# Kernel tuning notes

Hardware: AMD Instinct MI355X
Metric: run time of the kernel (lower is better)

## Reference

```python
import jax, jax.numpy as jnp
import numpy as np

B, L, D, H, M = 2, 512, 1024, 16, 16384
HD = D // H  # 64


def setup_inputs() -> dict:
    key = jax.random.key(0)
    ks = jax.random.split(key, 8)
    s = 0.02
    return {
        "x": jax.random.normal(ks[0], (B, L, D), dtype=jnp.float32),
        "mem_keys": jax.random.normal(ks[1], (M, HD), dtype=jnp.float32),
        "mem_values": jax.random.normal(ks[2], (M, HD), dtype=jnp.float32),
        "Wq": jax.random.normal(ks[3], (D, D), dtype=jnp.float32) * s,
        "bq": jnp.zeros((D,), jnp.float32),
        "Wk": jax.random.normal(ks[4], (D, D), dtype=jnp.float32) * s,
        "bk": jnp.zeros((D,), jnp.float32),
        "Wv": jax.random.normal(ks[5], (D, D), dtype=jnp.float32) * s,
        "bv": jnp.zeros((D,), jnp.float32),
        "Wo": jax.random.normal(ks[6], (D, D), dtype=jnp.float32) * s,
        "bo": jnp.zeros((D,), jnp.float32),
        "top_k": 8,
    }


def reference(x, mem_keys, mem_values, Wq, bq, Wk, bk, Wv, bv, Wo, bo, top_k):
    b, l, d = x.shape
    h, hd = H, d // H
    # Q/K/V projections -> [B, L, H, HD]
    q = (x @ Wq.T + bq).reshape(b, l, h, hd)
    k = (x @ Wk.T + bk).reshape(b, l, h, hd)
    v = (x @ Wv.T + bv).reshape(b, l, h, hd)

    # exact inner-product top-k memory search (FAISS equivalent) per (b, l, h) query
    q_flat = q.reshape(b * l * h, hd)
    sim = q_flat @ mem_keys.T                      # [B*L*H, M]
    idx = jax.lax.top_k(sim, top_k)[1]             # [B*L*H, K]
    # gather retrieved KV, lay out as memory-prefix along seq: [B, L*K, H, HD]
    m_k = mem_keys[idx].reshape(b, l, h, top_k, hd).transpose(0, 1, 3, 2, 4).reshape(b, l * top_k, h, hd)
    m_v = mem_values[idx].reshape(b, l, h, top_k, hd).transpose(0, 1, 3, 2, 4).reshape(b, l * top_k, h, hd)

    k_full = jnp.concatenate([m_k, k], axis=1)     # [B, Lm+L, H, HD]
    v_full = jnp.concatenate([m_v, v], axis=1)
    lm = l * top_k

    scale = 1.0 / np.sqrt(hd)
    scores = jnp.einsum("blhd,bmhd->bhlm", q, k_full) * scale
    # memory prefix always visible; local part causal (flash_attn bottom-right causal)
    i = jnp.arange(l)[:, None]
    j = jnp.arange(lm + l)[None, :]
    mask = (j < lm) | ((j - lm) <= i)              # [L, Lm+L]
    neg = jnp.finfo(scores.dtype).min
    attn = jax.nn.softmax(jnp.where(mask, scores, neg), axis=-1)
    out = jnp.einsum("bhlm,bmhd->blhd", attn, v_full).reshape(b, l, d)
    return out @ Wo.T + bo
```

## Files before the change

### kernel.cpp

```cpp
#include <hip/hip_runtime.h>

typedef __bf16 bf16_t;
typedef __bf16 bf16x8 __attribute__((ext_vector_type(8)));
typedef __bf16 bf16x4 __attribute__((ext_vector_type(4)));
typedef __bf16 bf16x2 __attribute__((ext_vector_type(2)));
typedef float f32x4 __attribute__((ext_vector_type(4)));

#define DEV __device__ __forceinline__
#define MFMA16 __builtin_amdgcn_mfma_f32_16x16x32_bf16

constexpr int Bb = 2, Ls = 512, Dd = 1024, Hh = 16, HD = 64, Mm = 16384, TK = 8;
constexpr int KSPLIT = 4;
constexpr int CAP = 40;
constexpr int NQ = Bb * Ls * Hh;
constexpr int CH = 3;

constexpr size_t OFF_QF   = 0;
constexpr size_t OFF_KF   = OFF_QF + (size_t)NQ * HD;
constexpr size_t OFF_VF   = OFF_KF + (size_t)NQ * HD;
constexpr size_t OFF_QH   = OFF_VF + (size_t)NQ * HD;
constexpr size_t OFF_QL   = OFF_QH + (size_t)NQ * HD / 2;
constexpr size_t OFF_KHG  = OFF_QL + (size_t)NQ * HD / 2;
constexpr size_t OFF_FCAND = OFF_KHG + (size_t)Mm * HD / 2;
constexpr size_t OFF_FCNT  = OFF_FCAND + (size_t)KSPLIT * NQ * CAP;
constexpr size_t OFF_F8   = OFF_FCNT + (size_t)KSPLIT * NQ;
constexpr size_t OFF_ML   = OFF_F8 + (size_t)NQ * TK;
constexpr size_t OFF_PA   = OFF_ML + (size_t)CH * NQ * 2;
constexpr size_t WS_ELEMS = OFF_PA + (size_t)CH * NQ * HD + 16;
constexpr size_t WS_BYTES = WS_ELEMS * 4;

DEV void ld8f(const float* p, float* dst) {
  float4 a = *(const float4*)p, b = *(const float4*)(p + 4);
  dst[0]=a.x; dst[1]=a.y; dst[2]=a.z; dst[3]=a.w;
  dst[4]=b.x; dst[5]=b.y; dst[6]=b.z; dst[7]=b.w;
}

DEV void split8(const float* av, bf16x8& hi, bf16x8& lo) {
#pragma unroll
  for (int j = 0; j < 8; ++j) {
    bf16_t h_ = (bf16_t)av[j];
    hi[j] = h_;
    lo[j] = (bf16_t)(av[j] - (float)h_);
  }
}

DEV bf16x8 ld8h(const bf16_t* p) {
  bf16x4 a = *(const bf16x4*)p;
  bf16x4 b = *(const bf16x4*)(p + 4);
  bf16x8 r;
#pragma unroll
  for (int i = 0; i < 4; ++i) { r[i] = a[i]; r[i + 4] = b[i]; }
  return r;
}

__global__ __launch_bounds__(256) void ws_sentinel(float* __restrict__ out, int n, float v) {
  int i = blockIdx.x * 256 + threadIdx.x;
  if (i < n) out[i] = v;
}

__global__ __launch_bounds__(256) void prep_keys(const float* __restrict__ mk,
                                                 bf16_t* __restrict__ khg) {
  const size_t i = ((size_t)blockIdx.x * 256 + threadIdx.x) * 8;
  float v[8]; ld8f(mk + i, v);
  bf16x8 h;
#pragma unroll
  for (int j = 0; j < 8; ++j) h[j] = (bf16_t)v[j];
  *(bf16x8*)(khg + i) = h;
}

__global__ __launch_bounds__(256) void qkv_mfma(
    const float* __restrict__ x,
    const float* __restrict__ Wq, const float* __restrict__ bq,
    const float* __restrict__ Wk, const float* __restrict__ bk,
    const float* __restrict__ Wv, const float* __restrict__ bv,
    float* __restrict__ qf, bf16_t* __restrict__ qh, bf16_t* __restrict__ ql,
    float* __restrict__ kf, float* __restrict__ vf) {
  const int z = blockIdx.z;
  const float* W    = (z == 0) ? Wq : ((z == 1) ? Wk : Wv);
  const float* bias = (z == 0) ? bq : ((z == 1) ? bk : bv);
  const int tid = threadIdx.x;
  const int lane = tid & 63, wv = tid >> 6;
  const int l15 = lane & 15, quad = lane >> 4;
  const int mrow = blockIdx.x * 64 + wv * 16 + l15;
  const int ncol0 = blockIdx.y * 64;
  f32x4 acc[4] = {};
  const size_t abase = (size_t)mrow * Dd + quad * 8;
  for (int kk = 0; kk < Dd; kk += 32) {
    float av[8]; ld8f(x + abase + kk, av);
    bf16x8 ahi, alo; split8(av, ahi, alo);
#pragma unroll
    for (int t = 0; t < 4; ++t) {
      float bv8[8]; ld8f(W + (size_t)(ncol0 + t * 16 + l15) * Dd + kk + quad * 8, bv8);
      bf16x8 bhi, blo; split8(bv8, bhi, blo);
      acc[t] = MFMA16(ahi, bhi, acc[t], 0, 0, 0);
      acc[t] = MFMA16(alo, bhi, acc[t], 0, 0, 0);
      acc[t] = MFMA16(ahi, blo, acc[t], 0, 0, 0);
    }
  }
#pragma unroll
  for (int t = 0; t < 4; ++t) {
    int col = ncol0 + t * 16 + l15;
    int h = col >> 6, hd = col & 63;
    float bb = bias[col];
#pragma unroll
    for (int r = 0; r < 4; ++r) {
      int row = blockIdx.x * 64 + wv * 16 + quad * 4 + r;
      int b = row >> 9, l = row & 511;
      float val = acc[t][r] + bb;
      size_t o = ((size_t)(b * Hh + h) * Ls + l) * HD + hd;
      if (z == 0) {
        qf[o] = val;
        bf16_t hv = (bf16_t)val;
        qh[o] = hv;
        ql[o] = (bf16_t)(val - (float)hv);
      } else if (z == 1) {
        kf[o] = val;
      } else {
        vf[o] = val;
      }
    }
  }
}

__global__ __launch_bounds__(256, 5) void topk_thresh(
    const bf16_t* __restrict__ qh, const bf16_t* __restrict__ khg,
    int* __restrict__ fcand, int* __restrict__ fcnt) {
  __shared__ __align__(16) float  W8[4][64][8];
  __shared__ float Tarr[64];
  __shared__ int   cntq[64];
  __shared__ int   Cand[64][CAP];

  const int tid = threadIdx.x;
  const int lane = tid & 63, w = tid >> 6;
  const int l15 = lane & 15, quad = lane >> 4;
  const int qbase = blockIdx.x * 64;
  const int split = blockIdx.y;
  const int key0 = split * (Mm / KSPLIT);
  constexpr int NT = (Mm / KSPLIT) / 64;

  bf16x8 bq[4][2];
#pragma unroll
  for (int g = 0; g < 4; ++g) {
    const bf16_t* qp = qh + (size_t)(qbase + g * 16 + l15) * HD + quad * 8;
    bq[g][0] = *(const bf16x8*)qp;
    bq[g][1] = *(const bf16x8*)(qp + 32);
  }

  const bf16_t* kbase = khg + (size_t)(key0 + w * 16 + l15) * HD + quad * 8;

  float s8[8];
#pragma unroll
  for (int r = 0; r < 8; ++r) s8[r] = -3.0e38f;

  bf16x8 a0 = *(const bf16x8*)(kbase);
  bf16x8 a1 = *(const bf16x8*)(kbase + 32);
  for (int tile = 0; tile < NT; ++tile) {
    const bf16_t* np = kbase + (size_t)((tile + 1 < NT) ? tile + 1 : 0) * (64 * HD);
    bf16x8 n0 = *(const bf16x8*)(np);
    bf16x8 n1 = *(const bf16x8*)(np + 32);
    float keep = -3.0e38f;
#pragma unroll
    for (int g = 0; g < 4; ++g) {
      f32x4 acc = {0.f, 0.f, 0.f, 0.f};
      acc = MFMA16(a0, bq[g][0], acc, 0, 0, 0);
      acc = MFMA16(a1, bq[g][1], acc, 0, 0, 0);
      float v = fmaxf(fmaxf(acc[0], acc[1]), fmaxf(acc[2], acc[3]));
      v = fmaxf(v, __shfl_xor(v, 16));
      v = fmaxf(v, __shfl_xor(v, 32));
      if (g == quad) keep = v;
    }
    if (keep > s8[7]) {
      s8[7] = keep;
#pragma unroll
      for (int p = 7; p > 0; --p)
        if (s8[p] > s8[p - 1]) { float t = s8[p]; s8[p] = s8[p - 1]; s8[p - 1] = t; }
    }
    a0 = n0; a1 = n1;
  }
  {
    float* dst = &W8[w][quad * 16 + l15][0];
#pragma unroll
    for (int r = 0; r < 8; ++r) dst[r] = s8[r];
  }
  __syncthreads();
  if (tid < 64) {
    float t8[8];
#pragma unroll
    for (int r = 0; r < 8; ++r) t8[r] = -3.0e38f;
#pragma unroll
    for (int wv2 = 0; wv2 < 4; ++wv2) {
      float4 u0 = *(const float4*)&W8[wv2][tid][0];
      float4 u1 = *(const float4*)&W8[wv2][tid][4];
      float vals[8] = {u0.x, u0.y, u0.z, u0.w, u1.x, u1.y, u1.z, u1.w};
#pragma unroll
      for (int r = 0; r < 8; ++r) {
        float v = vals[r];
        if (v > t8[7]) {
          t8[7] = v;
#pragma unroll
          for (int p = 7; p > 0; --p)
            if (t8[p] > t8[p - 1]) { float tt = t8[p]; t8[p] = t8[p - 1]; t8[p - 1] = tt; }
        }
      }
    }
    Tarr[tid] = t8[7];
    cntq[tid] = 0;
  }
  __syncthreads();
  float Tq[4];
#pragma unroll
  for (int g = 0; g < 4; ++g) Tq[g] = Tarr[g * 16 + l15];

  a0 = *(const bf16x8*)(kbase);
  a1 = *(const bf16x8*)(kbase + 32);
  for (int tile = 0; tile < NT; ++tile) {
    const bf16_t* np = kbase + (size_t)((tile + 1 < NT) ? tile + 1 : 0) * (64 * HD);
    bf16x8 n0 = *(const bf16x8*)(np);
    bf16x8 n1 = *(const bf16x8*)(np + 32);
#pragma unroll
    for (int g = 0; g < 4; ++g) {
      f32x4 acc = {0.f, 0.f, 0.f, 0.f};
      acc = MFMA16(a0, bq[g][0], acc, 0, 0, 0);
      acc = MFMA16(a1, bq[g][1], acc, 0, 0, 0);
      const int kb = key0 + tile * 64 + w * 16 + quad * 4;
      const int qq = g * 16 + l15;
#pragma unroll
      for (int r = 0; r < 4; ++r) {
        if (acc[r] >= Tq[g]) {
          int pos = atomicAdd(&cntq[qq], 1);
          if (pos < CAP) Cand[qq][pos] = kb + r;
        }
      }
    }
    a0 = n0; a1 = n1;
  }
  __syncthreads();
  if (tid < 64) {
    int c = cntq[tid];
    fcnt[(size_t)split * NQ + qbase + tid] = (c < CAP) ? c : CAP;
  }
  for (int i = tid; i < 64 * CAP; i += 256) {
    int q = i / CAP, s = i - q * CAP;
    fcand[((size_t)split * NQ + qbase + q) * CAP + s] = Cand[q][s];
  }
}

__global__ __launch_bounds__(64) void rescore8(
    const float* __restrict__ qf, const float* __restrict__ mk,
    const int* __restrict__ fcand, const int* __restrict__ fcnt,
    int* __restrict__ f8) {
  const int qid = blockIdx.x * 64 + threadIdx.x;
  float q[64];
#pragma unroll
  for (int c = 0; c < 16; ++c) {
    float4 v4 = *(const float4*)(qf + (size_t)qid * HD + 4 * c);
    q[4*c]=v4.x; q[4*c+1]=v4.y; q[4*c+2]=v4.z; q[4*c+3]=v4.w;
  }
  float sc[TK]; int id[TK];
#pragma unroll
  for (int r = 0; r < TK; ++r) { sc[r] = -3.0e38f; id[r] = 0x7fffffff; }
#pragma unroll 1
  for (int sp = 0; sp < KSPLIT; ++sp) {
    int cnt = fcnt[(size_t)sp * NQ + qid];
    if (cnt > CAP) cnt = CAP;
#pragma unroll 1
    for (int c = 0; c < cnt; ++c) {
      int kidx = fcand[((size_t)sp * NQ + qid) * CAP + c] & (Mm - 1);
      const float4* kr = (const float4*)(mk + (size_t)kidx * HD);
      float a0 = 0, a1 = 0, a2 = 0, a3 = 0;
#pragma unroll
      for (int cc = 0; cc < 16; ++cc) {
        float4 kv = kr[cc];
        a0 += q[4*cc]*kv.x; a1 += q[4*cc+1]*kv.y; a2 += q[4*cc+2]*kv.z; a3 += q[4*cc+3]*kv.w;
      }
      float s = (a0 + a1) + (a2 + a3);
      if (s > sc[TK - 1] || (s == sc[TK - 1] && kidx < id[TK - 1])) {
        sc[TK - 1] = s; id[TK - 1] = kidx;
#pragma unroll
        for (int p = TK - 1; p > 0; --p) {
          bool sw = (sc[p] > sc[p - 1]) || (sc[p] == sc[p - 1] && id[p] < id[p - 1]);
          if (sw) {
            float ts = sc[p]; sc[p] = sc[p - 1]; sc[p - 1] = ts;
            int   ti = id[p]; id[p] = id[p - 1]; id[p - 1] = ti;
          }
        }
      }
    }
  }
#pragma unroll
  for (int r = 0; r < TK; ++r) f8[(size_t)qid * TK + r] = id[r] & (Mm - 1);
}

__global__ __launch_bounds__(256) void flash_mfma(
    const bf16_t* __restrict__ qh, const bf16_t* __restrict__ ql,
    const float* __restrict__ kf, const float* __restrict__ vf,
    const float* __restrict__ mk, const float* __restrict__ mv,
    const int* __restrict__ f8, float* __restrict__ ml, float* __restrict__ pacc) {
  __shared__ __align__(16) bf16_t KH[64][72];
  __shared__ __align__(16) bf16_t KL[64][72];
  __shared__ __align__(16) bf16_t VTH[64][68];
  __shared__ __align__(16) bf16_t VTL[64][68];
  __shared__ __align__(16) bf16_t PH[64][72];
  __shared__ __align__(16) bf16_t PL[64][72];

  const int tid = threadIdx.x;
  const int lane = tid & 63, w = tid >> 6;
  const int l15 = lane & 15, quad = lane >> 4;
  const int qt = blockIdx.x, bh = blockIdx.y, chunk = blockIdx.z;
  const int il = qt * 64 + w * 16 + l15;
  const int qid = bh * Ls + il;
  const bf16x8 qh0 = *(const bf16x8*)(qh + (size_t)qid * HD + quad * 8);
  const bf16x8 qh1 = *(const bf16x8*)(qh + (size_t)qid * HD + 32 + quad * 8);
  const bf16x8 ql0 = *(const bf16x8*)(ql + (size_t)qid * HD + quad * 8);
  const bf16x8 ql1 = *(const bf16x8*)(ql + (size_t)qid * HD + 32 + quad * 8);

  f32x4 O[4] = {};
  float m = -3.0e38f, lsum = 0.f;
  const float scale = 0.125f;
  const int tbase = chunk * 24;
  const int nmem  = (chunk == 2) ? 16 : 24;
  const int ntiles = (chunk == 2) ? 17 + qt : 24;
  const int skey = tid >> 2, spart = tid & 3;
  const int kpair = tid & 31, dgroup = tid >> 5;

  float kreg[16], va[8], vb[8];
  auto stage_load = [&](int t) {
    const float *ks, *vsa, *vsb;
    if (chunk == 2 && t >= nmem) {
      int jlK = (t - nmem) * 64 + skey;
      ks = kf + ((size_t)bh * Ls + jlK) * HD + spart * 16;
      int jlV = (t - nmem) * 64 + 2 * kpair;
      vsa = vf + ((size_t)bh * Ls + jlV) * HD + dgroup * 8;
      vsb = vsa + HD;
    } else {
      int jgK = (tbase + t) * 64 + skey;
      int sK = f8[((size_t)bh * Ls + (jgK >> 3)) * TK + (jgK & 7)] & (Mm - 1);
      ks = mk + (size_t)sK * HD + spart * 16;
      int jgV = (tbase + t) * 64 + 2 * kpair;
      int2 s2 = *(const int2*)(f8 + ((size_t)bh * Ls + (jgV >> 3)) * TK + (jgV & 7));
      vsa = mv + (size_t)(s2.x & (Mm - 1)) * HD + dgroup * 8;
      vsb = mv + (size_t)(s2.y & (Mm - 1)) * HD + dgroup * 8;
    }
    ld8f(ks, kreg); ld8f(ks + 8, kreg + 8);
    ld8f(vsa, va);
    ld8f(vsb, vb);
  };
  stage_load(0);

  for (int tile = 0; tile < ntiles; ++tile) {
    const bool local_tile = (chunk == 2) && (tile >= nmem);
    __syncthreads();
    {
      bf16x8 h0, l0, h1, l1;
      split8(kreg, h0, l0); split8(kreg + 8, h1, l1);
      *(bf16x8*)&KH[skey][spart * 16]     = h0;
      *(bf16x8*)&KH[skey][spart * 16 + 8] = h1;
      *(bf16x8*)&KL[skey][spart * 16]     = l0;
      *(bf16x8*)&KL[skey][spart * 16 + 8] = l1;
#pragma unroll
      for (int j = 0; j < 8; ++j) {
        bf16_t ha = (bf16_t)va[j]; bf16_t la = (bf16_t)(va[j] - (float)ha);
        bf16_t hb = (bf16_t)vb[j]; bf16_t lb = (bf16_t)(vb[j] - (float)hb);
        const int d = dgroup * 8 + j;
        bf16x2 th; th[0] = ha; th[1] = hb;
        bf16x2 tl; tl[0] = la; tl[1] = lb;
        *(bf16x2*)&VTH[d][2 * kpair] = th;
        *(bf16x2*)&VTL[d][2 * kpair] = tl;
      }
    }
    __syncthreads();
    if (tile + 1 < ntiles) stage_load(tile + 1);

    f32x4 S[4];
    __builtin_amdgcn_s_setprio(1);
#pragma unroll
    for (int sub = 0; sub < 4; ++sub) {
      const bf16x8 ah0 = *(const bf16x8*)&KH[sub * 16 + l15][quad * 8];
      const bf16x8 ah1 = *(const bf16x8*)&KH[sub * 16 + l15][32 + quad * 8];
      const bf16x8 al0 = *(const bf16x8*)&KL[sub * 16 + l15][quad * 8];
      const bf16x8 al1 = *(const bf16x8*)&KL[sub * 16 + l15][32 + quad * 8];
      f32x4 acc = {0.f, 0.f, 0.f, 0.f};
      acc = MFMA16(ah0, qh0, acc, 0, 0, 0);
      acc = MFMA16(ah1, qh1, acc, 0, 0, 0);
      acc = MFMA16(al0, qh0, acc, 0, 0, 0);
      acc = MFMA16(al1, qh1, acc, 0, 0, 0);
      acc = MFMA16(ah0, ql0, acc, 0, 0, 0);
      acc = MFMA16(ah1, ql1, acc, 0, 0, 0);
#pragma unroll
      for (int r = 0; r < 4; ++r) {
        float sv = acc[r] * scale;
        if (local_tile && ((tile - nmem) * 64 + sub * 16 + quad * 4 + r) > il) sv = -3.0e38f;
        S[sub][r] = sv;
      }
    }
    __builtin_amdgcn_s_setprio(0);
    float tm = -3.0e38f;
#pragma unroll
    for (int sub = 0; sub < 4; ++sub)
#pragma unroll
      for (int r = 0; r < 4; ++r) tm = fmaxf(tm, S[sub][r]);
    tm = fmaxf(tm, __shfl_xor(tm, 16));
    tm = fmaxf(tm, __shfl_xor(tm, 32));
    float mnew = fmaxf(m, tm);
    float alpha = __expf(m - mnew);
    lsum *= alpha;
#pragma unroll
    for (int t = 0; t < 4; ++t) O[t] *= alpha;
    m = mnew;
#pragma unroll
    for (int sub = 0; sub < 4; ++sub) {
      bf16_t ph4[4], pl4[4];
#pragma unroll
      for (int r = 0; r < 4; ++r) {
        float p = __expf(S[sub][r] - mnew);
        lsum += p;
        bf16_t hv = (bf16_t)p;
        ph4[r] = hv;
        pl4[r] = (bf16_t)(p - (float)hv);
      }
      *(uint2*)&PH[w * 16 + l15][sub * 16 + quad * 4] = *(uint2*)ph4;
      *(uint2*)&PL[w * 16 + l15][sub * 16 + quad * 4] = *(uint2*)pl4;
    }
    const bf16x8 ph0 = *(const bf16x8*)&PH[w * 16 + l15][quad * 8];
    const bf16x8 ph1 = *(const bf16x8*)&PH[w * 16 + l15][32 + quad * 8];
    const bf16x8 pl0 = *(const bf16x8*)&PL[w * 16 + l15][quad * 8];
    const bf16x8 pl1 = *(const bf16x8*)&PL[w * 16 + l15][32 + quad * 8];
    __builtin_amdgcn_s_setprio(1);
#pragma unroll
    for (int t = 0; t < 4; ++t) {
      const bf16x8 vh0 = ld8h(&VTH[t * 16 + l15][quad * 8]);
      const bf16x8 vh1 = ld8h(&VTH[t * 16 + l15][32 + quad * 8]);
      const bf16x8 vl0 = ld8h(&VTL[t * 16 + l15][quad * 8]);
      const bf16x8 vl1 = ld8h(&VTL[t * 16 + l15][32 + quad * 8]);
      O[t] = MFMA16(vh0, ph0, O[t], 0, 0, 0);
      O[t] = MFMA16(vh1, ph1, O[t], 0, 0, 0);
      O[t] = MFMA16(vl0, ph0, O[t], 0, 0, 0);
      O[t] = MFMA16(vl1, ph1, O[t], 0, 0, 0);
      O[t] = MFMA16(vh0, pl0, O[t], 0, 0, 0);
      O[t] = MFMA16(vh1, pl1, O[t], 0, 0, 0);
    }
    __builtin_amdgcn_s_setprio(0);
  }
  lsum += __shfl_xor(lsum, 16);
  lsum += __shfl_xor(lsum, 32);
  if (quad == 0) {
    ml[((size_t)chunk * NQ + qid) * 2 + 0] = m;
    ml[((size_t)chunk * NQ + qid) * 2 + 1] = lsum;
  }
  float* pa = pacc + ((size_t)chunk * NQ + qid) * 64;
#pragma unroll
  for (int t = 0; t < 4; ++t) {
    float4 v4; v4.x = O[t][0]; v4.y = O[t][1]; v4.z = O[t][2]; v4.w = O[t][3];
    *(float4*)(pa + t * 16 + quad * 4) = v4;
  }
}

__global__ __launch_bounds__(256) void oproj_comb(
    const float* __restrict__ ml, const float* __restrict__ pacc,
    const float* __restrict__ Wo, const float* __restrict__ bo,
    float* __restrict__ out) {
  const int tid = threadIdx.x;
  const int lane = tid & 63, wv = tid >> 6;
  const int l15 = lane & 15, quad = lane >> 4;
  const int mrow = blockIdx.x * 64 + wv * 16 + l15;
  const int b = mrow >> 9, l = mrow & 511;
  const int ncol0 = blockIdx.y * 64;
  f32x4 acc[4] = {};
  for (int kk = 0; kk < Dd; kk += 32) {
    const int h = kk >> 6;
    const size_t qid = (size_t)(b * Hh + h) * Ls + l;
    float m0 = ml[qid * 2 + 0],                    l0 = ml[qid * 2 + 1];
    float m1 = ml[((size_t)NQ + qid) * 2 + 0],     l1 = ml[((size_t)NQ + qid) * 2 + 1];
    float m2 = ml[((size_t)2 * NQ + qid) * 2 + 0], l2 = ml[((size_t)2 * NQ + qid) * 2 + 1];
    float M = fmaxf(m0, fmaxf(m1, m2));
    float w0 = __expf(m0 - M), w1 = __expf(m1 - M), w2 = __expf(m2 - M);
    float inv = 1.f / (w0 * l0 + w1 * l1 + w2 * l2);
    const int d0 = (kk & 63) + quad * 8;
    float a0v[8], a1v[8], a2v[8], av[8];
    ld8f(pacc + qid * 64 + d0, a0v);
    ld8f(pacc + ((size_t)NQ + qid) * 64 + d0, a1v);
    ld8f(pacc + ((size_t)2 * NQ + qid) * 64 + d0, a2v);
#pragma unroll
    for (int j = 0; j < 8; ++j) av[j] = (w0 * a0v[j] + w1 * a1v[j] + w2 * a2v[j]) * inv;
    bf16x8 ahi, alo; split8(av, ahi, alo);
#pragma unroll
    for (int t = 0; t < 4; ++t) {
      float wv8[8]; ld8f(Wo + (size_t)(ncol0 + t * 16 + l15) * Dd + kk + quad * 8, wv8);
      bf16x8 whi, wlo; split8(wv8, whi, wlo);
      acc[t] = MFMA16(ahi, whi, acc[t], 0, 0, 0);
      acc[t] = MFMA16(alo, whi, acc[t], 0, 0, 0);
      acc[t] = MFMA16(ahi, wlo, acc[t], 0, 0, 0);
    }
  }
#pragma unroll
  for (int t = 0; t < 4; ++t) {
    int col = ncol0 + t * 16 + l15;
    float bb = bo[col];
#pragma unroll
    for (int r = 0; r < 4; ++r) {
      int row = blockIdx.x * 64 + wv * 16 + quad * 4 + r;
      out[(size_t)row * Dd + col] = acc[t][r] + bb;
    }
  }
}

extern "C" void kernel_launch(void* const* d_in, const int* in_sizes, int n_in,
                              void* d_out, int out_size, void* d_ws, size_t ws_size,
                              hipStream_t stream) {
  (void)in_sizes; (void)n_in;
  const float* x  = (const float*)d_in[0];
  const float* mk = (const float*)d_in[1];
  const float* mv = (const float*)d_in[2];
  const float* Wq = (const float*)d_in[3];
  const float* bq = (const float*)d_in[4];
  const float* Wk = (const float*)d_in[5];
  const float* bk = (const float*)d_in[6];
  const float* Wv = (const float*)d_in[7];
  const float* bv = (const float*)d_in[8];
  const float* Wo = (const float*)d_in[9];
  const float* bo = (const float*)d_in[10];
  float* ws = (float*)d_ws;

  if (ws_size < WS_BYTES) {
    float v = (float)(ws_size >> 20) + 0.5f;
    ws_sentinel<<<(out_size + 255) / 256, 256, 0, stream>>>((float*)d_out, out_size, v);
    return;
  }

  float*  QF    = ws + OFF_QF;
  float*  KF    = ws + OFF_KF;
  float*  VF    = ws + OFF_VF;
  bf16_t* QH    = (bf16_t*)(ws + OFF_QH);
  bf16_t* QL    = (bf16_t*)(ws + OFF_QL);
  bf16_t* KHG   = (bf16_t*)(ws + OFF_KHG);
  int*    FCAND = (int*)(ws + OFF_FCAND);
  int*    FCNT  = (int*)(ws + OFF_FCNT);
  int*    F8    = (int*)(ws + OFF_F8);
  float*  ML    = ws + OFF_ML;
  float*  PA    = ws + OFF_PA;

  prep_keys<<<(Mm * HD) / (256 * 8), 256, 0, stream>>>(mk, KHG);
  qkv_mfma<<<dim3(16, 16, 3), 256, 0, stream>>>(x, Wq, bq, Wk, bk, Wv, bv, QF, QH, QL, KF, VF);
  topk_thresh<<<dim3(NQ / 64, KSPLIT), 256, 0, stream>>>(QH, KHG, FCAND, FCNT);
  rescore8<<<NQ / 64, 64, 0, stream>>>(QF, mk, FCAND, FCNT, F8);
  flash_mfma<<<dim3(8, 32, 3), 256, 0, stream>>>(QH, QL, KF, VF, mk, mv, F8, ML, PA);
  oproj_comb<<<dim3(16, 16), 256, 0, stream>>>(ML, PA, Wo, bo, (float*)d_out);
}
```

Before: 596.4 us.

## Pre-split K/V into bf16 hi/lo, stage weights in LDS, split top-k keys further

The QKV and output projections now convert each weight tile to bf16 hi/lo once into double-buffered shared memory, so the four waves no longer each reload and re-split it. Local K/V and the memory keys/values are pre-split into bf16 hi/lo arrays (memory values in a new prep kernel placed after rescore, aliased into the candidate buffer), so the flash kernel loads half the bytes and skips the conversion. The top-k threshold kernel gains a second grid axis that halves each key range, and candidate lists are merged with global atomic offsets into zero-initialised counts. The extra launch, the extra syncs in the GEMMs, and per-block thresholds computed over fewer keys add cost and could change how many candidates are kept.

```diff
diff --git a/kernel.cpp b/kernel.cpp
--- a/kernel.cpp
+++ b/kernel.cpp
@@ -16,9 +16,11 @@
 constexpr int CH = 3;
 
 constexpr size_t OFF_QF   = 0;
-constexpr size_t OFF_KF   = OFF_QF + (size_t)NQ * HD;
-constexpr size_t OFF_VF   = OFF_KF + (size_t)NQ * HD;
-constexpr size_t OFF_QH   = OFF_VF + (size_t)NQ * HD;
+constexpr size_t OFF_KH2  = OFF_QF + (size_t)NQ * HD;
+constexpr size_t OFF_KL2  = OFF_KH2 + (size_t)NQ * HD / 2;
+constexpr size_t OFF_VH2  = OFF_KL2 + (size_t)NQ * HD / 2;
+constexpr size_t OFF_VL2  = OFF_VH2 + (size_t)NQ * HD / 2;
+constexpr size_t OFF_QH   = OFF_VL2 + (size_t)NQ * HD / 2;
 constexpr size_t OFF_QL   = OFF_QH + (size_t)NQ * HD / 2;
 constexpr size_t OFF_KHG  = OFF_QL + (size_t)NQ * HD / 2;
 constexpr size_t OFF_FCAND = OFF_KHG + (size_t)Mm * HD / 2;
@@ -29,6 +31,11 @@
 constexpr size_t WS_ELEMS = OFF_PA + (size_t)CH * NQ * HD + 16;
 constexpr size_t WS_BYTES = WS_ELEMS * 4;
 
+constexpr size_t OFF_GKL = OFF_FCAND;
+constexpr size_t OFF_GVH = OFF_GKL + (size_t)Mm * HD / 2;
+constexpr size_t OFF_GVL = OFF_GVH + (size_t)Mm * HD / 2;
+static_assert(OFF_GVL + (size_t)Mm * HD / 2 <= OFF_FCNT, "alias fits in FCAND");
+
 DEV void ld8f(const float* p, float* dst) {
   float4 a = *(const float4*)p, b = *(const float4*)(p + 4);
   dst[0]=a.x; dst[1]=a.y; dst[2]=a.z; dst[3]=a.w;
@@ -59,13 +66,38 @@
 }
 
 __global__ __launch_bounds__(256) void prep_keys(const float* __restrict__ mk,
-                                                 bf16_t* __restrict__ khg) {
-  const size_t i = ((size_t)blockIdx.x * 256 + threadIdx.x) * 8;
+                                                 bf16_t* __restrict__ khg,
+                                                 int* __restrict__ fcnt) {
+  const int gid = blockIdx.x * 256 + threadIdx.x;
+  if (gid < KSPLIT * NQ) fcnt[gid] = 0;
+  const size_t i = (size_t)gid * 8;
   float v[8]; ld8f(mk + i, v);
   bf16x8 h;
 #pragma unroll
   for (int j = 0; j < 8; ++j) h[j] = (bf16_t)v[j];
   *(bf16x8*)(khg + i) = h;
+}
+
+__global__ __launch_bounds__(256) void prep_kv2(const float* __restrict__ mk,
+                                                const float* __restrict__ mv,
+                                                bf16_t* __restrict__ gkl,
+                                                bf16_t* __restrict__ gvh,
+                                                bf16_t* __restrict__ gvl) {
+  const size_t i = ((size_t)blockIdx.x * 256 + threadIdx.x) * 8;
+  float a[8]; ld8f(mk + i, a);
+  float b[8]; ld8f(mv + i, b);
+  bf16x8 kl, vh, vl;
+#pragma unroll
+  for (int j = 0; j < 8; ++j) {
+    bf16_t kh_ = (bf16_t)a[j];
+    kl[j] = (bf16_t)(a[j] - (float)kh_);
+    bf16_t vh_ = (bf16_t)b[j];
+    vh[j] = vh_;
+    vl[j] = (bf16_t)(b[j] - (float)vh_);
+  }
+  *(bf16x8*)(gkl + i) = kl;
+  *(bf16x8*)(gvh + i) = vh;
+  *(bf16x8*)(gvl + i) = vl;
 }
 
 __global__ __launch_bounds__(256) void qkv_mfma(
@@ -73,8 +105,11 @@
     const float* __restrict__ Wq, const float* __restrict__ bq,
     const float* __restrict__ Wk, const float* __restrict__ bk,
     const float* __restrict__ Wv, const float* __restrict__ bv,
-    float* __restrict__ qf, bf16_t* __restrict__ qh, bf16_t* __restrict__ ql,
-    float* __restrict__ kf, float* __restrict__ vf) {
+    float* __restrict__ qf, bf16_t* __restrict__ qhp, bf16_t* __restrict__ qlp,
+    bf16_t* __restrict__ kh2, bf16_t* __restrict__ kl2,
+    bf16_t* __restrict__ vh2, bf16_t* __restrict__ vl2) {
+  __shared__ __align__(16) bf16_t WHs[2][64][40];
+  __shared__ __align__(16) bf16_t WLs[2][64][40];
   const int z = blockIdx.z;
   const float* W    = (z == 0) ? Wq : ((z == 1) ? Wk : Wv);
   const float* bias = (z == 0) ? bq : ((z == 1) ? bk : bv);
@@ -83,19 +118,36 @@
   const int l15 = lane & 15, quad = lane >> 4;
   const int mrow = blockIdx.x * 64 + wv * 16 + l15;
   const int ncol0 = blockIdx.y * 64;
+  const int srow = tid >> 2, scol = (tid & 3) * 8;
   f32x4 acc[4] = {};
   const size_t abase = (size_t)mrow * Dd + quad * 8;
+  const size_t wbase = (size_t)(ncol0 + srow) * Dd + scol;
+  {
+    float wv8[8]; ld8f(W + wbase, wv8);
+    bf16x8 h, l; split8(wv8, h, l);
+    *(bf16x8*)&WHs[0][srow][scol] = h;
+    *(bf16x8*)&WLs[0][srow][scol] = l;
+  }
+  int p = 0;
   for (int kk = 0; kk < Dd; kk += 32) {
+    __syncthreads();
+    if (kk + 32 < Dd) {
+      float wv8[8]; ld8f(W + wbase + kk + 32, wv8);
+      bf16x8 h, l; split8(wv8, h, l);
+      *(bf16x8*)&WHs[p ^ 1][srow][scol] = h;
+      *(bf16x8*)&WLs[p ^ 1][srow][scol] = l;
+    }
     float av[8]; ld8f(x + abase + kk, av);
     bf16x8 ahi, alo; split8(av, ahi, alo);
 #pragma unroll
     for (int t = 0; t < 4; ++t) {
-      float bv8[8]; ld8f(W + (size_t)(ncol0 + t * 16 + l15) * Dd + kk + quad * 8, bv8);
-      bf16x8 bhi, blo; split8(bv8, bhi, blo);
+      const bf16x8 bhi = *(const bf16x8*)&WHs[p][t * 16 + l15][quad * 8];
+      const bf16x8 blo = *(const bf16x8*)&WLs[p][t * 16 + l15][quad * 8];
       acc[t] = MFMA16(ahi, bhi, acc[t], 0, 0, 0);
       acc[t] = MFMA16(alo, bhi, acc[t], 0, 0, 0);
       acc[t] = MFMA16(ahi, blo, acc[t], 0, 0, 0);
     }
+    p ^= 1;
   }
 #pragma unroll
   for (int t = 0; t < 4; ++t) {
@@ -111,23 +163,25 @@
       if (z == 0) {
         qf[o] = val;
         bf16_t hv = (bf16_t)val;
-        qh[o] = hv;
-        ql[o] = (bf16_t)(val - (float)hv);
-      } else if (z == 1) {
-        kf[o] = val;
+        qhp[o] = hv;
+        qlp[o] = (bf16_t)(val - (float)hv);
       } else {
-        vf[o] = val;
-      }
-    }
-  }
-}
-
-__global__ __launch_bounds__(256, 5) void topk_thresh(
+        bf16_t hv = (bf16_t)val;
+        bf16_t lv = (bf16_t)(val - (float)hv);
+        if (z == 1) { kh2[o] = hv; kl2[o] = lv; }
+        else        { vh2[o] = hv; vl2[o] = lv; }
+      }
+    }
+  }
+}
+
+__global__ __launch_bounds__(256, 8) void topk_thresh(
     const bf16_t* __restrict__ qh, const bf16_t* __restrict__ khg,
     int* __restrict__ fcand, int* __restrict__ fcnt) {
   __shared__ __align__(16) float  W8[4][64][8];
   __shared__ float Tarr[64];
   __shared__ int   cntq[64];
+  __shared__ int   baseq[64];
   __shared__ int   Cand[64][CAP];
 
   const int tid = threadIdx.x;
@@ -135,8 +189,8 @@
   const int l15 = lane & 15, quad = lane >> 4;
   const int qbase = blockIdx.x * 64;
   const int split = blockIdx.y;
-  const int key0 = split * (Mm / KSPLIT);
-  constexpr int NT = (Mm / KSPLIT) / 64;
+  const int key0 = split * (Mm / KSPLIT) + blockIdx.z * (Mm / KSPLIT / 2);
+  constexpr int NT = (Mm / KSPLIT / 2) / 64;
 
   bf16x8 bq[4][2];
 #pragma unroll
@@ -236,12 +290,17 @@
   }
   __syncthreads();
   if (tid < 64) {
-    int c = cntq[tid];
-    fcnt[(size_t)split * NQ + qbase + tid] = (c < CAP) ? c : CAP;
-  }
+    int c = cntq[tid]; if (c > CAP) c = CAP;
+    cntq[tid] = c;
+    baseq[tid] = atomicAdd(&fcnt[(size_t)split * NQ + qbase + tid], c);
+  }
+  __syncthreads();
   for (int i = tid; i < 64 * CAP; i += 256) {
     int q = i / CAP, s = i - q * CAP;
-    fcand[((size_t)split * NQ + qbase + q) * CAP + s] = Cand[q][s];
+    if (s < cntq[q]) {
+      int pos = baseq[q] + s;
+      if (pos < CAP) fcand[((size_t)split * NQ + qbase + q) * CAP + pos] = Cand[q][s];
+    }
   }
 }
 
@@ -293,8 +352,10 @@
 
 __global__ __launch_bounds__(256) void flash_mfma(
     const bf16_t* __restrict__ qh, const bf16_t* __restrict__ ql,
-    const float* __restrict__ kf, const float* __restrict__ vf,
-    const float* __restrict__ mk, const float* __restrict__ mv,
+    const bf16_t* __restrict__ kh2, const bf16_t* __restrict__ kl2,
+    const bf16_t* __restrict__ vh2, const bf16_t* __restrict__ vl2,
+    const bf16_t* __restrict__ khg, const bf16_t* __restrict__ gkl,
+    const bf16_t* __restrict__ gvh, const bf16_t* __restrict__ gvl,
     const int* __restrict__ f8, float* __restrict__ ml, float* __restrict__ pacc) {
   __shared__ __align__(16) bf16_t KH[64][72];
   __shared__ __align__(16) bf16_t KL[64][72];
@@ -323,49 +384,58 @@
   const int skey = tid >> 2, spart = tid & 3;
   const int kpair = tid & 31, dgroup = tid >> 5;
 
-  float kreg[16], va[8], vb[8];
+  bf16x8 kA0, kA1, kB0, kB1;
+  bf16x8 vha, vhb, vla, vlb;
+  bf16x2 vth[8], vtl[8];
   auto stage_load = [&](int t) {
-    const float *ks, *vsa, *vsb;
+    const bf16_t *ksh, *ksl, *vah, *val_, *vbh, *vbl;
     if (chunk == 2 && t >= nmem) {
       int jlK = (t - nmem) * 64 + skey;
-      ks = kf + ((size_t)bh * Ls + jlK) * HD + spart * 16;
+      size_t ro = ((size_t)bh * Ls + jlK) * HD + spart * 16;
+      ksh = kh2 + ro; ksl = kl2 + ro;
       int jlV = (t - nmem) * 64 + 2 * kpair;
-      vsa = vf + ((size_t)bh * Ls + jlV) * HD + dgroup * 8;
-      vsb = vsa + HD;
+      size_t ra = ((size_t)bh * Ls + jlV) * HD + dgroup * 8;
+      vah = vh2 + ra;      val_ = vl2 + ra;
+      vbh = vh2 + ra + HD; vbl  = vl2 + ra + HD;
     } else {
       int jgK = (tbase + t) * 64 + skey;
       int sK = f8[((size_t)bh * Ls + (jgK >> 3)) * TK + (jgK & 7)] & (Mm - 1);
-      ks = mk + (size_t)sK * HD + spart * 16;
+      size_t ro = (size_t)sK * HD + spart * 16;
+      ksh = khg + ro; ksl = gkl + ro;
       int jgV = (tbase + t) * 64 + 2 * kpair;
       int2 s2 = *(const int2*)(f8 + ((size_t)bh * Ls + (jgV >> 3)) * TK + (jgV & 7));
-      vsa = mv + (size_t)(s2.x & (Mm - 1)) * HD + dgroup * 8;
-      vsb = mv + (size_t)(s2.y & (Mm - 1)) * HD + dgroup * 8;
-    }
-    ld8f(ks, kreg); ld8f(ks + 8, kreg + 8);
-    ld8f(vsa, va);
-    ld8f(vsb, vb);
+      size_t ra = (size_t)(s2.x & (Mm - 1)) * HD + dgroup * 8;
+      size_t rb = (size_t)(s2.y & (Mm - 1)) * HD + dgroup * 8;
+      vah = gvh + ra; val_ = gvl + ra;
+      vbh = gvh + rb; vbl  = gvl + rb;
+    }
+    kA0 = *(const bf16x8*)ksh; kA1 = *(const bf16x8*)(ksh + 8);
+    kB0 = *(const bf16x8*)ksl; kB1 = *(const bf16x8*)(ksl + 8);
+    vha = *(const bf16x8*)vah; vla = *(const bf16x8*)val_;
+    vhb = *(const bf16x8*)vbh; vlb = *(const bf16x8*)vbl;
+  };
+  auto pack_v = [&]() {
+#pragma unroll
+    for (int j = 0; j < 8; ++j) {
+      vth[j][0] = vha[j]; vth[j][1] = vhb[j];
+      vtl[j][0] = vla[j]; vtl[j][1] = vlb[j];
+    }
   };
   stage_load(0);
+  pack_v();
 
   for (int tile = 0; tile < ntiles; ++tile) {
     const bool local_tile = (chunk == 2) && (tile >= nmem);
     __syncthreads();
     {
-      bf16x8 h0, l0, h1, l1;
-      split8(kreg, h0, l0); split8(kreg + 8, h1, l1);
-      *(bf16x8*)&KH[skey][spart * 16]     = h0;
-      *(bf16x8*)&KH[skey][spart * 16 + 8] = h1;
-      *(bf16x8*)&KL[skey][spart * 16]     = l0;
-      *(bf16x8*)&KL[skey][spart * 16 + 8] = l1;
+      *(bf16x8*)&KH[skey][spart * 16]     = kA0;
+      *(bf16x8*)&KH[skey][spart * 16 + 8] = kA1;
+      *(bf16x8*)&KL[skey][spart * 16]     = kB0;
+      *(bf16x8*)&KL[skey][spart * 16 + 8] = kB1;
 #pragma unroll
       for (int j = 0; j < 8; ++j) {
-        bf16_t ha = (bf16_t)va[j]; bf16_t la = (bf16_t)(va[j] - (float)ha);
-        bf16_t hb = (bf16_t)vb[j]; bf16_t lb = (bf16_t)(vb[j] - (float)hb);
-        const int d = dgroup * 8 + j;
-        bf16x2 th; th[0] = ha; th[1] = hb;
-        bf16x2 tl; tl[0] = la; tl[1] = lb;
-        *(bf16x2*)&VTH[d][2 * kpair] = th;
-        *(bf16x2*)&VTL[d][2 * kpair] = tl;
+        *(bf16x2*)&VTH[dgroup * 8 + j][2 * kpair] = vth[j];
+        *(bf16x2*)&VTL[dgroup * 8 + j][2 * kpair] = vtl[j];
       }
     }
     __syncthreads();
@@ -440,6 +510,7 @@
       O[t] = MFMA16(vh1, pl1, O[t], 0, 0, 0);
     }
     __builtin_amdgcn_s_setprio(0);
+    if (tile + 1 < ntiles) pack_v();
   }
   lsum += __shfl_xor(lsum, 16);
   lsum += __shfl_xor(lsum, 32);
@@ -459,22 +530,40 @@
     const float* __restrict__ ml, const float* __restrict__ pacc,
     const float* __restrict__ Wo, const float* __restrict__ bo,
     float* __restrict__ out) {
+  __shared__ __align__(16) bf16_t WHs[2][64][40];
+  __shared__ __align__(16) bf16_t WLs[2][64][40];
   const int tid = threadIdx.x;
   const int lane = tid & 63, wv = tid >> 6;
   const int l15 = lane & 15, quad = lane >> 4;
   const int mrow = blockIdx.x * 64 + wv * 16 + l15;
   const int b = mrow >> 9, l = mrow & 511;
   const int ncol0 = blockIdx.y * 64;
+  const int srow = tid >> 2, scol = (tid & 3) * 8;
+  const size_t wbase = (size_t)(ncol0 + srow) * Dd + scol;
   f32x4 acc[4] = {};
+  {
+    float wv8[8]; ld8f(Wo + wbase, wv8);
+    bf16x8 h, l2; split8(wv8, h, l2);
+    *(bf16x8*)&WHs[0][srow][scol] = h;
+    *(bf16x8*)&WLs[0][srow][scol] = l2;
+  }
+  int p = 0;
   for (int kk = 0; kk < Dd; kk += 32) {
+    __syncthreads();
+    if (kk + 32 < Dd) {
+      float wv8[8]; ld8f(Wo + wbase + kk + 32, wv8);
+      bf16x8 h, l2; split8(wv8, h, l2);
+      *(bf16x8*)&WHs[p ^ 1][srow][scol] = h;
+      *(bf16x8*)&WLs[p ^ 1][srow][scol] = l2;
+    }
     const int h = kk >> 6;
     const size_t qid = (size_t)(b * Hh + h) * Ls + l;
     float m0 = ml[qid * 2 + 0],                    l0 = ml[qid * 2 + 1];
     float m1 = ml[((size_t)NQ + qid) * 2 + 0],     l1 = ml[((size_t)NQ + qid) * 2 + 1];
-    float m2 = ml[((size_t)2 * NQ + qid) * 2 + 0], l2 = ml[((size_t)2 * NQ + qid) * 2 + 1];
+    float m2 = ml[((size_t)2 * NQ + qid) * 2 + 0], l2v = ml[((size_t)2 * NQ + qid) * 2 + 1];
     float M = fmaxf(m0, fmaxf(m1, m2));
     float w0 = __expf(m0 - M), w1 = __expf(m1 - M), w2 = __expf(m2 - M);
-    float inv = 1.f / (w0 * l0 + w1 * l1 + w2 * l2);
+    float inv = 1.f / (w0 * l0 + w1 * l1 + w2 * l2v);
     const int d0 = (kk & 63) + quad * 8;
     float a0v[8], a1v[8], a2v[8], av[8];
     ld8f(pacc + qid * 64 + d0, a0v);
@@ -485,12 +574,13 @@
     bf16x8 ahi, alo; split8(av, ahi, alo);
 #pragma unroll
     for (int t = 0; t < 4; ++t) {
-      float wv8[8]; ld8f(Wo + (size_t)(ncol0 + t * 16 + l15) * Dd + kk + quad * 8, wv8);
-      bf16x8 whi, wlo; split8(wv8, whi, wlo);
+      const bf16x8 whi = *(const bf16x8*)&WHs[p][t * 16 + l15][quad * 8];
+      const bf16x8 wlo = *(const bf16x8*)&WLs[p][t * 16 + l15][quad * 8];
       acc[t] = MFMA16(ahi, whi, acc[t], 0, 0, 0);
       acc[t] = MFMA16(alo, whi, acc[t], 0, 0, 0);
       acc[t] = MFMA16(ahi, wlo, acc[t], 0, 0, 0);
     }
+    p ^= 1;
   }
 #pragma unroll
   for (int t = 0; t < 4; ++t) {
@@ -528,8 +618,10 @@
   }
 
   float*  QF    = ws + OFF_QF;
-  float*  KF    = ws + OFF_KF;
-  float*  VF    = ws + OFF_VF;
+  bf16_t* KH2   = (bf16_t*)(ws + OFF_KH2);
+  bf16_t* KL2   = (bf16_t*)(ws + OFF_KL2);
+  bf16_t* VH2   = (bf16_t*)(ws + OFF_VH2);
+  bf16_t* VL2   = (bf16_t*)(ws + OFF_VL2);
   bf16_t* QH    = (bf16_t*)(ws + OFF_QH);
   bf16_t* QL    = (bf16_t*)(ws + OFF_QL);
   bf16_t* KHG   = (bf16_t*)(ws + OFF_KHG);
@@ -538,11 +630,17 @@
   int*    F8    = (int*)(ws + OFF_F8);
   float*  ML    = ws + OFF_ML;
   float*  PA    = ws + OFF_PA;
-
-  prep_keys<<<(Mm * HD) / (256 * 8), 256, 0, stream>>>(mk, KHG);
-  qkv_mfma<<<dim3(16, 16, 3), 256, 0, stream>>>(x, Wq, bq, Wk, bk, Wv, bv, QF, QH, QL, KF, VF);
-  topk_thresh<<<dim3(NQ / 64, KSPLIT), 256, 0, stream>>>(QH, KHG, FCAND, FCNT);
+  bf16_t* GKL   = (bf16_t*)(ws + OFF_GKL);
+  bf16_t* GVH   = (bf16_t*)(ws + OFF_GVH);
+  bf16_t* GVL   = (bf16_t*)(ws + OFF_GVL);
+
+  prep_keys<<<(Mm * HD) / (256 * 8), 256, 0, stream>>>(mk, KHG, FCNT);
+  qkv_mfma<<<dim3(16, 16, 3), 256, 0, stream>>>(x, Wq, bq, Wk, bk, Wv, bv,
+                                                QF, QH, QL, KH2, KL2, VH2, VL2);
+  topk_thresh<<<dim3(NQ / 64, KSPLIT, 2), 256, 0, stream>>>(QH, KHG, FCAND, FCNT);
   rescore8<<<NQ / 64, 64, 0, stream>>>(QF, mk, FCAND, FCNT, F8);
-  flash_mfma<<<dim3(8, 32, 3), 256, 0, stream>>>(QH, QL, KF, VF, mk, mv, F8, ML, PA);
+  prep_kv2<<<(Mm * HD) / (256 * 8), 256, 0, stream>>>(mk, mv, GKL, GVH, GVL);
+  flash_mfma<<<dim3(8, 32, 3), 256, 0, stream>>>(QH, QL, KH2, KL2, VH2, VL2,
+                                                 KHG, GKL, GVH, GVL, F8, ML, PA);
   oproj_comb<<<dim3(16, 16), 256, 0, stream>>>(ML, PA, Wo, bo, (float*)d_out);
 }
```

Result: slower. 766.5 us (+28.5%).
